# Optimization experiments

Measured on AMD Instinct MI355X. Metric: run time of the kernel, lower is better.

The kernel has to match this reference:

```python
import jax, jax.numpy as jnp
import numpy as np

K = 3          # kernel size (both dims)
PAD = 1        # padding used both for offset_mask conv and deform_conv2d
KK = K * K


def setup_inputs() -> dict:
    key = jax.random.key(0)
    k0, k1, k2, k3, k4 = jax.random.split(key, 5)
    B, C, H, W, O = 8, 64, 64, 64, 64
    input_feat = jax.random.normal(k0, (B, C, H, W), jnp.float32)
    degrad_inter = jax.random.normal(k1, (B, C, H, W), jnp.float32)
    stdv = 1.0 / np.sqrt(C * K * K)
    weight = jax.random.uniform(k2, (O, C, K, K), jnp.float32, -stdv, stdv)
    # small-magnitude offset/mask conv params -> realistic small learned offsets
    om_weight = jax.random.normal(k3, (3 * KK, 2 * C, K, K), jnp.float32) * 0.01
    om_bias = jax.random.normal(k4, (3 * KK,), jnp.float32) * 0.01
    return {"input_feat": input_feat, "degrad_inter": degrad_inter,
            "weight": weight, "om_weight": om_weight, "om_bias": om_bias}


def _conv2d(x, w, b):
    out = jax.lax.conv_general_dilated(
        x, w, window_strides=(1, 1), padding=((PAD, PAD), (PAD, PAD)),
        dimension_numbers=("NCHW", "OIHW", "NCHW"))
    return out + b[None, :, None, None]


def _deform_conv2d(x, offset, mask, weight):
    # x: (B,C,H,W); offset: (B,2*KK,H,W) with channel 2k=dy_k, 2k+1=dx_k;
    # mask: (B,KK,H,W); weight: (O,C,K,K). stride=1, padding=PAD, dilation=1.
    B, C, H, W = x.shape
    O = weight.shape[0]
    off = offset.reshape(B, KK, 2, H, W)
    dy, dx = off[:, :, 0], off[:, :, 1]                       # (B,KK,H,W)

    ky, kx = jnp.meshgrid(jnp.arange(K), jnp.arange(K), indexing="ij")
    ky = ky.reshape(KK).astype(x.dtype)
    kx = kx.reshape(KK).astype(x.dtype)
    hh = jnp.arange(H, dtype=x.dtype)
    ww = jnp.arange(W, dtype=x.dtype)
    # absolute fractional sample locations: (B,KK,H,W)
    y = hh[None, None, :, None] - PAD + ky[None, :, None, None] + dy
    xq = ww[None, None, None, :] - PAD + kx[None, :, None, None] + dx

    y0 = jnp.floor(y).astype(jnp.int32)
    x0 = jnp.floor(xq).astype(jnp.int32)
    y1, x1 = y0 + 1, x0 + 1
    wy = y - y0.astype(x.dtype)
    wx = xq - x0.astype(x.dtype)

    x_flat = x.reshape(B, C, H * W)

    def gather(yi, xi):
        valid = (yi >= 0) & (yi < H) & (xi >= 0) & (xi < W)
        idx = jnp.clip(yi, 0, H - 1) * W + jnp.clip(xi, 0, W - 1)  # (B,KK,H,W)
        vals = jax.vmap(lambda im, ix: im[:, ix])(x_flat, idx)     # (B,C,KK,H,W)
        return vals * valid[:, None].astype(x.dtype)

    wy_ = wy[:, None]  # (B,1,KK,H,W)
    wx_ = wx[:, None]
    sampled = (gather(y0, x0) * (1 - wy_) * (1 - wx_)
               + gather(y0, x1) * (1 - wy_) * wx_
               + gather(y1, x0) * wy_ * (1 - wx_)
               + gather(y1, x1) * wy_ * wx_)                       # (B,C,KK,H,W)
    sampled = sampled * mask[:, None]
    return jnp.einsum("bckhw,ock->bohw", sampled, weight.reshape(O, C, KK))


def reference(input_feat, degrad_inter, weight, om_weight, om_bias):
    concat = jnp.concatenate([input_feat, degrad_inter], axis=1)
    om = _conv2d(concat, om_weight, om_bias)                       # (B,3*KK,H,W)
    off1, off2, mask = jnp.split(om, 3, axis=1)
    offset = jnp.concatenate([off1, off2], axis=1)                 # (B,2*KK,H,W)
    mask = jax.nn.sigmoid(mask)                                    # (B,KK,H,W)
    return _deform_conv2d(input_feat, offset, mask, weight)
```

## Files before the change

### kernel.cpp

```cpp
#include <hip/hip_runtime.h>
#include <math.h>

#define WO_PK_OFF 36864
#define CATT_OFF  73728

typedef short  short8  __attribute__((ext_vector_type(8)));
typedef float  float4v __attribute__((ext_vector_type(4)));

static __device__ __forceinline__ short f2bf(float f) {
    unsigned int u = __builtin_bit_cast(unsigned int, f);
    u += 0x7FFFu + ((u >> 16) & 1u);
    return (short)(u >> 16);
}
static __device__ __forceinline__ float bf2f(unsigned short u) {
    return __builtin_bit_cast(float, (unsigned int)u << 16);
}

__global__ __launch_bounds__(256) void prep_transpose(
    const float* __restrict__ feat, const float* __restrict__ deg,
    const float* __restrict__ weight, const float* __restrict__ om_weight,
    unsigned short* __restrict__ catT,
    short* __restrict__ wd_pk, short* __restrict__ wo_pk)
{
    __shared__ unsigned short T[64 * 136];
    const int tid = threadIdx.x;
    if (blockIdx.x < 512) {
        const int b = blockIdx.x >> 6, h = blockIdx.x & 63;
        const int lane = tid & 63, wv = tid >> 6;
#pragma unroll
        for (int cc = 0; cc < 32; cc++) {
            int c = wv * 32 + cc;
            const float* src = (c < 64)
                ? (feat + (size_t)(b * 64 + c) * 4096)
                : (deg  + (size_t)(b * 64 + (c - 64)) * 4096);
            T[lane * 136 + c] = (unsigned short)f2bf(src[h * 64 + lane]);
        }
        __syncthreads();
        const int px = tid >> 2, seg = tid & 3;
        unsigned short* dst =
            catT + (size_t)(b * 4096 + h * 64 + px) * 128 + seg * 32;
#pragma unroll
        for (int j = 0; j < 4; j++)
            *(uint4*)(dst + j * 8) = *(const uint4*)&T[px * 136 + seg * 32 + j * 8];
    } else {
        int idx = (blockIdx.x - 512) * 256 + tid;
        if (idx < 36864) {
            int j = idx & 7, o = (idx >> 3) & 63;
            int lq = (idx >> 9) & 3, ks = idx >> 11;
            int t = ks >> 1, c = (ks & 1) * 32 + lq * 8 + j;
            wd_pk[idx] = f2bf(weight[(o * 64 + c) * 9 + t]);
        } else {
            int e = idx - 36864;
            int j = e & 7, oc = (e >> 3) & 31;
            int lq = (e >> 8) & 3, ks2 = e >> 10;
            int quarter = ks2 / 9, t = ks2 - quarter * 9;
            int cg = quarter * 32 + lq * 8 + j;
            wo_pk[e] = (oc < 27) ? f2bf(om_weight[(oc * 128 + cg) * 9 + t])
                                 : (short)0;
        }
    }
}

__global__ __launch_bounds__(256, 2) void fused_kernel(
    const unsigned short* __restrict__ catT, const short* __restrict__ wd_pk,
    const short* __restrict__ wo_pk, const float* __restrict__ om_bias,
    float* __restrict__ out)
{
    __shared__ short8 Lraw[2304];
    short8* A1 = Lraw;
    float*  Tw = (float*)Lraw;
    short8* A3 = Lraw + 576;

    const int tid = threadIdx.x;
    const int lane = tid & 63, wv = tid >> 6;
    const int l16 = lane & 15, lq = lane >> 4;
    const int b = blockIdx.x & 7;
    const int h = blockIdx.x >> 3;
    const int w0 = wv << 4;
    const int pxx = w0 + l16;
    const unsigned short* cb = catT + (size_t)b * 4096 * 128;
    const short8 zf = {0, 0, 0, 0, 0, 0, 0, 0};

    auto loadB1 = [&](int q, int t) -> short8 {
        int ky = t / 3, kx = t - ky * 3;
        int yy = h - 1 + ky, xx = pxx - 1 + kx;
        bool ok = (yy >= 0) & (yy <= 63) & (xx >= 0) & (xx <= 63);
        int yc = min(max(yy, 0), 63), xc = min(max(xx, 0), 63);
        short8 v = *(const short8*)(cb + (yc * 64 + xc) * 128
                                       + q * 32 + lq * 8);
        return ok ? v : zf;
    };

    {
        const short8* src = (const short8*)wo_pk;
        short8 g0 = src[tid], g1 = src[tid + 256];
        short8 g2 = src[tid + 512], g3 = src[tid + 768];
        short8 g4 = zf; if (tid < 128) g4 = src[tid + 1024];
        A1[tid] = g0; A1[tid + 256] = g1; A1[tid + 512] = g2; A1[tid + 768] = g3;
        if (tid < 128) A1[tid + 1024] = g4;
    }
    __syncthreads();

    float4v oacc0 = {0.f, 0.f, 0.f, 0.f};
    float4v oacc1 = {0.f, 0.f, 0.f, 0.f};
#pragma unroll
    for (int q = 0; q < 4; q++) {
        const int bufo = (q & 1) * 1152;
        short8 g0 = zf, g1 = zf, g2 = zf, g3 = zf, g4 = zf;
        if (q < 3) {
            const short8* src = (const short8*)(wo_pk + (q + 1) * 9216);
            g0 = src[tid]; g1 = src[tid + 256];
            g2 = src[tid + 512]; g3 = src[tid + 768];
            if (tid < 128) g4 = src[tid + 1024];
        }
        short8 b0 = loadB1(q, 0), b1 = loadB1(q, 1), b2 = loadB1(q, 2);
        short8 b3 = loadB1(q, 3), b4 = loadB1(q, 4), b5 = loadB1(q, 5);
        short8 b6 = loadB1(q, 6), b7 = loadB1(q, 7), b8 = loadB1(q, 8);
#define PH1_STEP(SL, BREG) { \
        short8 af0 = A1[bufo + (SL) * 128 + lq * 32 + l16]; \
        short8 af1 = A1[bufo + (SL) * 128 + lq * 32 + 16 + l16]; \
        oacc0 = __builtin_amdgcn_mfma_f32_16x16x32_bf16(af0, BREG, oacc0, 0, 0, 0); \
        oacc1 = __builtin_amdgcn_mfma_f32_16x16x32_bf16(af1, BREG, oacc1, 0, 0, 0); }
        PH1_STEP(0, b0) PH1_STEP(1, b1) PH1_STEP(2, b2)
        PH1_STEP(3, b3) PH1_STEP(4, b4) PH1_STEP(5, b5)
        PH1_STEP(6, b6) PH1_STEP(7, b7) PH1_STEP(8, b8)
#undef PH1_STEP
        if (q < 3) {
            const int bufn = ((q + 1) & 1) * 1152;
            A1[bufn + tid] = g0; A1[bufn + tid + 256] = g1;
            A1[bufn + tid + 512] = g2; A1[bufn + tid + 768] = g3;
            if (tid < 128) A1[bufn + tid + 1024] = g4;
        }
        __syncthreads();
    }

    float* Twv = Tw + wv * 576;
#pragma unroll
    for (int r = 0; r < 4; r++) {
        Twv[l16 * 36 + lq * 4 + r]      = oacc0[r];
        Twv[l16 * 36 + 16 + lq * 4 + r] = oacc1[r];
    }
    short8 s0 = ((const short8*)wd_pk)[tid];
    short8 s1 = ((const short8*)wd_pk)[tid + 256];
    __syncthreads();
    float omv[28];
#pragma unroll
    for (int jj = 0; jj < 7; jj++) {
        float4v tv = *(const float4v*)&Twv[l16 * 36 + jj * 4];
        omv[jj * 4 + 0] = tv[0]; omv[jj * 4 + 1] = tv[1];
        omv[jj * 4 + 2] = tv[2]; omv[jj * 4 + 3] = tv[3];
    }
#pragma unroll
    for (int j = 0; j < 27; j++) omv[j] += om_bias[j];
    A3[tid] = s0; A3[tid + 256] = s1;
    __syncthreads();

    float4v acc0 = {0.f, 0.f, 0.f, 0.f}, acc1 = {0.f, 0.f, 0.f, 0.f};
    float4v acc2 = {0.f, 0.f, 0.f, 0.f}, acc3 = {0.f, 0.f, 0.f, 0.f};
#pragma unroll
    for (int t = 0; t < 9; t++) {
        const int bo = (t & 1) * 512;
        short8 g0 = zf, g1 = zf;
        if (t < 8) {
            const short8* src = (const short8*)wd_pk + (t + 1) * 512;
            g0 = src[tid]; g1 = src[tid + 256];
        }
        const int ky = t / 3, kx = t - ky * 3;
        float dy = omv[2 * t], dx = omv[2 * t + 1];
        float mm = 1.f / (1.f + __expf(-omv[18 + t]));
        float yf = (float)(h - 1 + ky) + dy;
        float xf = (float)(pxx - 1 + kx) + dx;
        float fy = floorf(yf), fx = floorf(xf);
        int y0 = (int)fy, x0 = (int)fx;
        float wy = yf - fy, wx = xf - fx;
        bool vy0 = (y0 >= 0) & (y0 < 64);
        bool vy1 = (y0 >= -1) & (y0 < 63);
        bool vx0 = (x0 >= 0) & (x0 < 64);
        bool vx1 = (x0 >= -1) & (x0 < 63);
        float a0 = (1.f - wy) * mm, a1 = wy * mm;
        float W00 = a0 * (1.f - wx) * (float)(vy0 & vx0);
        float W01 = a0 * wx         * (float)(vy0 & vx1);
        float W10 = a1 * (1.f - wx) * (float)(vy1 & vx0);
        float W11 = a1 * wx         * (float)(vy1 & vx1);
        int iy0 = min(max(y0, 0), 63),     ix0 = min(max(x0, 0), 63);
        int iy1 = min(max(y0 + 1, 0), 63), ix1 = min(max(x0 + 1, 0), 63);
        const unsigned short* p00 = cb + (iy0 * 64 + ix0) * 128 + lq * 8;
        const unsigned short* p01 = cb + (iy0 * 64 + ix1) * 128 + lq * 8;
        const unsigned short* p10 = cb + (iy1 * 64 + ix0) * 128 + lq * 8;
        const unsigned short* p11 = cb + (iy1 * 64 + ix1) * 128 + lq * 8;
        short8 c00a = *(const short8*)p00,        c01a = *(const short8*)p01;
        short8 c10a = *(const short8*)p10,        c11a = *(const short8*)p11;
        short8 c00b = *(const short8*)(p00 + 32), c01b = *(const short8*)(p01 + 32);
        short8 c10b = *(const short8*)(p10 + 32), c11b = *(const short8*)(p11 + 32);
        short8 d00 = A3[bo + lq * 64 + l16];
        short8 d01 = A3[bo + lq * 64 + 16 + l16];
        short8 d02 = A3[bo + lq * 64 + 32 + l16];
        short8 d03 = A3[bo + lq * 64 + 48 + l16];
        short8 d10 = A3[bo + 256 + lq * 64 + l16];
        short8 d11 = A3[bo + 256 + lq * 64 + 16 + l16];
        short8 d12 = A3[bo + 256 + lq * 64 + 32 + l16];
        short8 d13 = A3[bo + 256 + lq * 64 + 48 + l16];
        short8 bfr0, bfr1;
#pragma unroll
        for (int j = 0; j < 8; j++) {
            float v0 = W00 * bf2f((unsigned short)c00a[j])
                     + W01 * bf2f((unsigned short)c01a[j])
                     + W10 * bf2f((unsigned short)c10a[j])
                     + W11 * bf2f((unsigned short)c11a[j]);
            float v1 = W00 * bf2f((unsigned short)c00b[j])
                     + W01 * bf2f((unsigned short)c01b[j])
                     + W10 * bf2f((unsigned short)c10b[j])
                     + W11 * bf2f((unsigned short)c11b[j]);
            bfr0[j] = f2bf(v0);
            bfr1[j] = f2bf(v1);
        }
        acc0 = __builtin_amdgcn_mfma_f32_16x16x32_bf16(d00, bfr0, acc0, 0, 0, 0);
        acc1 = __builtin_amdgcn_mfma_f32_16x16x32_bf16(d01, bfr0, acc1, 0, 0, 0);
        acc2 = __builtin_amdgcn_mfma_f32_16x16x32_bf16(d02, bfr0, acc2, 0, 0, 0);
        acc3 = __builtin_amdgcn_mfma_f32_16x16x32_bf16(d03, bfr0, acc3, 0, 0, 0);
        acc0 = __builtin_amdgcn_mfma_f32_16x16x32_bf16(d10, bfr1, acc0, 0, 0, 0);
        acc1 = __builtin_amdgcn_mfma_f32_16x16x32_bf16(d11, bfr1, acc1, 0, 0, 0);
        acc2 = __builtin_amdgcn_mfma_f32_16x16x32_bf16(d12, bfr1, acc2, 0, 0, 0);
        acc3 = __builtin_amdgcn_mfma_f32_16x16x32_bf16(d13, bfr1, acc3, 0, 0, 0);
        if (t < 8) {
            const int bn = ((t + 1) & 1) * 512;
            A3[bn + tid] = g0; A3[bn + tid + 256] = g1;
        }
        __syncthreads();
    }

    float* ob = out + (size_t)(b * 64) * 4096 + h * 64 + w0 + l16;
#pragma unroll
    for (int r = 0; r < 4; r++) ob[(lq * 4 + r) * 4096]      = acc0[r];
#pragma unroll
    for (int r = 0; r < 4; r++) ob[(16 + lq * 4 + r) * 4096] = acc1[r];
#pragma unroll
    for (int r = 0; r < 4; r++) ob[(32 + lq * 4 + r) * 4096] = acc2[r];
#pragma unroll
    for (int r = 0; r < 4; r++) ob[(48 + lq * 4 + r) * 4096] = acc3[r];
}

extern "C" void kernel_launch(void* const* d_in, const int* in_sizes, int n_in,
                              void* d_out, int out_size, void* d_ws, size_t ws_size,
                              hipStream_t stream)
{
    const float* feat      = (const float*)d_in[0];
    const float* deg       = (const float*)d_in[1];
    const float* weight    = (const float*)d_in[2];
    const float* om_weight = (const float*)d_in[3];
    const float* om_bias   = (const float*)d_in[4];
    float* out = (float*)d_out;
    short* wss = (short*)d_ws;
    unsigned short* catT = (unsigned short*)(wss + CATT_OFF);

    hipLaunchKernelGGL(prep_transpose, dim3(800), dim3(256), 0, stream,
                       feat, deg, weight, om_weight, catT,
                       wss, wss + WO_PK_OFF);
    hipLaunchKernelGGL(fused_kernel,   dim3(512), dim3(256), 0, stream,
                       catT, wss, wss + WO_PK_OFF, om_bias, out);
}
```

Before: 115.6 us.

## Merge prep and fused kernels into one cooperative kernel with grid sync

Combines the transpose/weight-packing prep kernel and the main deformable-conv kernel into a single cooperative launch. A grid-wide sync separates the bf16 transpose phase from the compute phase, and weight packing is spread across the first 288 blocks. The deform phase now reads the packed weight fragments straight from global memory (L2) instead of double-buffering them through LDS with per-tap barriers. This removes one kernel launch and the per-tap syncthreads, but adds the cost of a grid barrier, requires all 512 blocks to be co-resident, and makes the weight loads depend on cache hits.

```diff
diff --git a/kernel.cpp b/kernel.cpp
--- a/kernel.cpp
+++ b/kernel.cpp
@@ -1,5 +1,8 @@
 #include <hip/hip_runtime.h>
+#include <hip/hip_cooperative_groups.h>
 #include <math.h>
+
+namespace cg = cooperative_groups;
 
 #define WO_PK_OFF 36864
 #define CATT_OFF  73728
@@ -16,17 +19,23 @@
     return __builtin_bit_cast(float, (unsigned int)u << 16);
 }
 
-__global__ __launch_bounds__(256) void prep_transpose(
+__global__ __launch_bounds__(256, 2) void mono_kernel(
     const float* __restrict__ feat, const float* __restrict__ deg,
     const float* __restrict__ weight, const float* __restrict__ om_weight,
+    const float* __restrict__ om_bias,
     unsigned short* __restrict__ catT,
-    short* __restrict__ wd_pk, short* __restrict__ wo_pk)
+    short* __restrict__ wd_pk, short* __restrict__ wo_pk,
+    float* __restrict__ out)
 {
-    __shared__ unsigned short T[64 * 136];
+    __shared__ short8 Lraw[2304];
     const int tid = threadIdx.x;
-    if (blockIdx.x < 512) {
-        const int b = blockIdx.x >> 6, h = blockIdx.x & 63;
-        const int lane = tid & 63, wv = tid >> 6;
+    const int lane = tid & 63, wv = tid >> 6;
+    const int b = blockIdx.x & 7;
+    const int h = blockIdx.x >> 3;
+    const short8 zf = {0, 0, 0, 0, 0, 0, 0, 0};
+
+    {
+        unsigned short* T = (unsigned short*)Lraw;
 #pragma unroll
         for (int cc = 0; cc < 32; cc++) {
             int c = wv * 32 + cc;
@@ -35,6 +44,23 @@
                 : (deg  + (size_t)(b * 64 + (c - 64)) * 4096);
             T[lane * 136 + c] = (unsigned short)f2bf(src[h * 64 + lane]);
         }
+        if (blockIdx.x < 288) {
+            int idx = blockIdx.x * 256 + tid;
+            if (idx < 36864) {
+                int j = idx & 7, o = (idx >> 3) & 63;
+                int lq2 = (idx >> 9) & 3, ks = idx >> 11;
+                int t = ks >> 1, c = (ks & 1) * 32 + lq2 * 8 + j;
+                wd_pk[idx] = f2bf(weight[(o * 64 + c) * 9 + t]);
+            } else {
+                int e = idx - 36864;
+                int j = e & 7, oc = (e >> 3) & 31;
+                int lq2 = (e >> 8) & 3, ks2 = e >> 10;
+                int quarter = ks2 / 9, t = ks2 - quarter * 9;
+                int cg2 = quarter * 32 + lq2 * 8 + j;
+                wo_pk[e] = (oc < 27) ? f2bf(om_weight[(oc * 128 + cg2) * 9 + t])
+                                     : (short)0;
+            }
+        }
         __syncthreads();
         const int px = tid >> 2, seg = tid & 3;
         unsigned short* dst =
@@ -42,44 +68,16 @@
 #pragma unroll
         for (int j = 0; j < 4; j++)
             *(uint4*)(dst + j * 8) = *(const uint4*)&T[px * 136 + seg * 32 + j * 8];
-    } else {
-        int idx = (blockIdx.x - 512) * 256 + tid;
-        if (idx < 36864) {
-            int j = idx & 7, o = (idx >> 3) & 63;
-            int lq = (idx >> 9) & 3, ks = idx >> 11;
-            int t = ks >> 1, c = (ks & 1) * 32 + lq * 8 + j;
-            wd_pk[idx] = f2bf(weight[(o * 64 + c) * 9 + t]);
-        } else {
-            int e = idx - 36864;
-            int j = e & 7, oc = (e >> 3) & 31;
-            int lq = (e >> 8) & 3, ks2 = e >> 10;
-            int quarter = ks2 / 9, t = ks2 - quarter * 9;
-            int cg = quarter * 32 + lq * 8 + j;
-            wo_pk[e] = (oc < 27) ? f2bf(om_weight[(oc * 128 + cg) * 9 + t])
-                                 : (short)0;
-        }
-    }
-}
-
-__global__ __launch_bounds__(256, 2) void fused_kernel(
-    const unsigned short* __restrict__ catT, const short* __restrict__ wd_pk,
-    const short* __restrict__ wo_pk, const float* __restrict__ om_bias,
-    float* __restrict__ out)
-{
-    __shared__ short8 Lraw[2304];
-    short8* A1 = Lraw;
-    float*  Tw = (float*)Lraw;
-    short8* A3 = Lraw + 576;
-
-    const int tid = threadIdx.x;
-    const int lane = tid & 63, wv = tid >> 6;
+    }
+    __threadfence();
+    cg::this_grid().sync();
+
     const int l16 = lane & 15, lq = lane >> 4;
-    const int b = blockIdx.x & 7;
-    const int h = blockIdx.x >> 3;
     const int w0 = wv << 4;
     const int pxx = w0 + l16;
     const unsigned short* cb = catT + (size_t)b * 4096 * 128;
-    const short8 zf = {0, 0, 0, 0, 0, 0, 0, 0};
+    short8* A1 = Lraw;
+    float*  Tw = (float*)Lraw;
 
     auto loadB1 = [&](int q, int t) -> short8 {
         int ky = t / 3, kx = t - ky * 3;
@@ -140,8 +138,6 @@
         Twv[l16 * 36 + lq * 4 + r]      = oacc0[r];
         Twv[l16 * 36 + 16 + lq * 4 + r] = oacc1[r];
     }
-    short8 s0 = ((const short8*)wd_pk)[tid];
-    short8 s1 = ((const short8*)wd_pk)[tid + 256];
     __syncthreads();
     float omv[28];
 #pragma unroll
@@ -152,19 +148,11 @@
     }
 #pragma unroll
     for (int j = 0; j < 27; j++) omv[j] += om_bias[j];
-    A3[tid] = s0; A3[tid + 256] = s1;
-    __syncthreads();
 
     float4v acc0 = {0.f, 0.f, 0.f, 0.f}, acc1 = {0.f, 0.f, 0.f, 0.f};
     float4v acc2 = {0.f, 0.f, 0.f, 0.f}, acc3 = {0.f, 0.f, 0.f, 0.f};
 #pragma unroll
     for (int t = 0; t < 9; t++) {
-        const int bo = (t & 1) * 512;
-        short8 g0 = zf, g1 = zf;
-        if (t < 8) {
-            const short8* src = (const short8*)wd_pk + (t + 1) * 512;
-            g0 = src[tid]; g1 = src[tid + 256];
-        }
         const int ky = t / 3, kx = t - ky * 3;
         float dy = omv[2 * t], dx = omv[2 * t + 1];
         float mm = 1.f / (1.f + __expf(-omv[18 + t]));
@@ -192,14 +180,16 @@
         short8 c10a = *(const short8*)p10,        c11a = *(const short8*)p11;
         short8 c00b = *(const short8*)(p00 + 32), c01b = *(const short8*)(p01 + 32);
         short8 c10b = *(const short8*)(p10 + 32), c11b = *(const short8*)(p11 + 32);
-        short8 d00 = A3[bo + lq * 64 + l16];
-        short8 d01 = A3[bo + lq * 64 + 16 + l16];
-        short8 d02 = A3[bo + lq * 64 + 32 + l16];
-        short8 d03 = A3[bo + lq * 64 + 48 + l16];
-        short8 d10 = A3[bo + 256 + lq * 64 + l16];
-        short8 d11 = A3[bo + 256 + lq * 64 + 16 + l16];
-        short8 d12 = A3[bo + 256 + lq * 64 + 32 + l16];
-        short8 d13 = A3[bo + 256 + lq * 64 + 48 + l16];
+        const short* D0 = wd_pk + (size_t)((2 * t) * 4 + lq) * 512;
+        const short* D1 = wd_pk + (size_t)((2 * t + 1) * 4 + lq) * 512;
+        short8 d00 = *(const short8*)(D0 + l16 * 8);
+        short8 d01 = *(const short8*)(D0 + (16 + l16) * 8);
+        short8 d02 = *(const short8*)(D0 + (32 + l16) * 8);
+        short8 d03 = *(const short8*)(D0 + (48 + l16) * 8);
+        short8 d10 = *(const short8*)(D1 + l16 * 8);
+        short8 d11 = *(const short8*)(D1 + (16 + l16) * 8);
+        short8 d12 = *(const short8*)(D1 + (32 + l16) * 8);
+        short8 d13 = *(const short8*)(D1 + (48 + l16) * 8);
         short8 bfr0, bfr1;
 #pragma unroll
         for (int j = 0; j < 8; j++) {
@@ -222,11 +212,6 @@
         acc1 = __builtin_amdgcn_mfma_f32_16x16x32_bf16(d11, bfr1, acc1, 0, 0, 0);
         acc2 = __builtin_amdgcn_mfma_f32_16x16x32_bf16(d12, bfr1, acc2, 0, 0, 0);
         acc3 = __builtin_amdgcn_mfma_f32_16x16x32_bf16(d13, bfr1, acc3, 0, 0, 0);
-        if (t < 8) {
-            const int bn = ((t + 1) & 1) * 512;
-            A3[bn + tid] = g0; A3[bn + tid + 256] = g1;
-        }
-        __syncthreads();
     }
 
     float* ob = out + (size_t)(b * 64) * 4096 + h * 64 + w0 + l16;
@@ -251,11 +236,15 @@
     const float* om_bias   = (const float*)d_in[4];
     float* out = (float*)d_out;
     short* wss = (short*)d_ws;
+    short* wd_pk = wss;
+    short* wo_pk = wss + WO_PK_OFF;
     unsigned short* catT = (unsigned short*)(wss + CATT_OFF);
 
-    hipLaunchKernelGGL(prep_transpose, dim3(800), dim3(256), 0, stream,
-                       feat, deg, weight, om_weight, catT,
-                       wss, wss + WO_PK_OFF);
-    hipLaunchKernelGGL(fused_kernel,   dim3(512), dim3(256), 0, stream,
-                       catT, wss, wss + WO_PK_OFF, om_bias, out);
-}
+    void* args[] = {
+        (void*)&feat, (void*)&deg, (void*)&weight, (void*)&om_weight,
+        (void*)&om_bias, (void*)&catT, (void*)&wd_pk, (void*)&wo_pk,
+        (void*)&out
+    };
+    hipLaunchCooperativeKernel((const void*)mono_kernel,
+                               dim3(512), dim3(256), args, 0, stream);
+}
```

After: 264.3 us. 129% more time.
